# Kernel tuning notes

Measured on AMD Instinct MI355X. Metric: run time of the kernel, lower is better.

The kernel has to match this reference:

```python
import jax, jax.numpy as jnp
import numpy as np


def setup_inputs() -> dict:
    key = jax.random.key(0)
    kq, kk, kwq, kwk, kwv = jax.random.split(key, 5)
    B, T, C, H = 16, 2048, 1024, 64
    q = jax.random.normal(kq, (B, T, C), dtype=jnp.float32)
    k = jax.random.normal(kk, (B, T, C), dtype=jnp.float32)
    s = 1.0 / np.sqrt(C)
    Wq = jax.random.normal(kwq, (C, H), dtype=jnp.float32) * s
    Wk = jax.random.normal(kwk, (C, H), dtype=jnp.float32) * s
    Wv = jax.random.normal(kwv, (C, H), dtype=jnp.float32) * s
    return {"q": q, "k": k, "Wq": Wq, "Wk": Wk, "Wv": Wv}


def reference(q, k, Wq, Wk, Wv):
    # q, k: (B, T, C); projections are bias-free C -> head_size H
    Q = q @ Wq            # (B, T, H)
    K = k @ Wk            # (B, T, H)
    V = k @ Wv            # (B, T, H)
    T = q.shape[1]
    # NOTE: original scales by input dim C (q.shape[-1]), not head_size
    scale = q.shape[-1] ** (-0.5)
    wei = jnp.einsum('bth,bsh->bts', Q, K) * scale   # (B, T, T)
    causal = jnp.tril(jnp.ones((T, T), dtype=bool))
    wei = jnp.where(causal, wei, -jnp.inf)
    wei = jax.nn.softmax(wei, axis=-1)
    # dropout rate is 0.0 -> identity at inference
    out = jnp.einsum('bts,bsh->bth', wei, V)         # (B, T, H)
    return out
```

## Files before the change

### kernel.cpp

```cpp
#include <hip/hip_runtime.h>
#include <hip/hip_bf16.h>

typedef __bf16 bf16;
typedef __bf16 bf16x8 __attribute__((ext_vector_type(8)));
typedef float f32x4 __attribute__((ext_vector_type(4)));

#define MFMA_16x16x32(A, B, C) __builtin_amdgcn_mfma_f32_16x16x32_bf16(A, B, C, 0, 0, 0)

static_assert(sizeof(bf16x8) == 16, "bf16x8 must be 16B");

__global__ __launch_bounds__(256) void wtrans_kernel(
    const float* __restrict__ Wq, const float* __restrict__ Wk,
    const float* __restrict__ Wv, bf16* __restrict__ Wt)
{
  int idx = blockIdx.x * 256 + threadIdx.x;
  int p = idx >> 16;
  int rem = idx & 65535;
  int h = rem >> 10;
  int c = rem & 1023;
  const float* W = (p == 0) ? Wq : (p == 1) ? Wk : Wv;
  Wt[idx] = (bf16)W[c * 64 + h];
}

__global__ __launch_bounds__(256) void proj_kernel(
    const float* __restrict__ qin, const float* __restrict__ kin,
    const bf16* __restrict__ Wt,
    bf16* __restrict__ Qb, bf16* __restrict__ Kb, bf16* __restrict__ Vtb)
{
  const int p = blockIdx.y;
  const int m0 = blockIdx.x * 128;
  const float* A = (p == 0) ? qin : kin;
  const int nmat = (p == 0) ? 1 : 2;

  __shared__ __align__(16) bf16 Bs[2][64][80];

  const int tid = threadIdx.x;
  const int lane = tid & 63;
  const int w = tid >> 6;
  const int g = lane >> 4;
  const int r = lane & 15;

  f32x4 acc[2][2][4];
  #pragma unroll
  for (int mt = 0; mt < 2; mt++)
    #pragma unroll
    for (int rf = 0; rf < 2; rf++)
      #pragma unroll
      for (int cf = 0; cf < 4; cf++)
        acc[mt][rf][cf] = (f32x4){0.f, 0.f, 0.f, 0.f};

  const int bh = tid >> 2;
  const int bc = (tid & 3) * 16;

  for (int k0 = 0; k0 < 1024; k0 += 64) {
    #pragma unroll
    for (int mt = 0; mt < 2; mt++) {
      if (mt < nmat) {
        const bf16* src = Wt + (size_t)((p == 0) ? 0 : 1 + mt) * 65536
                          + (size_t)bh * 1024 + k0 + bc;
        *(bf16x8*)&Bs[mt][bh][bc]     = *(const bf16x8*)src;
        *(bf16x8*)&Bs[mt][bh][bc + 8] = *(const bf16x8*)(src + 8);
      }
    }
    __syncthreads();

    bf16x8 af[2][2];
    #pragma unroll
    for (int rf = 0; rf < 2; rf++) {
      const float* ap = A + (size_t)(m0 + w * 32 + rf * 16 + r) * 1024 + k0 + g * 8;
      float4 a0 = *(const float4*)(ap);
      float4 a1 = *(const float4*)(ap + 4);
      float4 a2 = *(const float4*)(ap + 32);
      float4 a3 = *(const float4*)(ap + 36);
      af[rf][0] = (bf16x8){(bf16)a0.x, (bf16)a0.y, (bf16)a0.z, (bf16)a0.w,
                           (bf16)a1.x, (bf16)a1.y, (bf16)a1.z, (bf16)a1.w};
      af[rf][1] = (bf16x8){(bf16)a2.x, (bf16)a2.y, (bf16)a2.z, (bf16)a2.w,
                           (bf16)a3.x, (bf16)a3.y, (bf16)a3.z, (bf16)a3.w};
    }

    #pragma unroll
    for (int mt = 0; mt < 2; mt++) {
      if (mt < nmat) {
        #pragma unroll
        for (int cf = 0; cf < 4; cf++) {
          bf16x8 b0 = *(const bf16x8*)&Bs[mt][cf * 16 + r][g * 8];
          bf16x8 b1 = *(const bf16x8*)&Bs[mt][cf * 16 + r][32 + g * 8];
          #pragma unroll
          for (int rf = 0; rf < 2; rf++) {
            acc[mt][rf][cf] = MFMA_16x16x32(af[rf][0], b0, acc[mt][rf][cf]);
            acc[mt][rf][cf] = MFMA_16x16x32(af[rf][1], b1, acc[mt][rf][cf]);
          }
        }
      }
    }
    __syncthreads();
  }

  #pragma unroll
  for (int rf = 0; rf < 2; rf++) {
    #pragma unroll
    for (int cf = 0; cf < 4; cf++) {
      #pragma unroll
      for (int j = 0; j < 4; j++) {
        int rg = m0 + w * 32 + rf * 16 + g * 4 + j;
        int col = cf * 16 + r;
        if (p == 0) {
          Qb[(size_t)rg * 64 + col] = (bf16)acc[0][rf][cf][j];
        } else {
          Kb[(size_t)rg * 64 + col] = (bf16)acc[0][rf][cf][j];
          int bb = rg >> 11, t = rg & 2047;
          Vtb[(size_t)(bb * 64 + col) * 2048 + t] = (bf16)acc[1][rf][cf][j];
        }
      }
    }
  }
}

__global__ __launch_bounds__(256) void attn_kernel(
    const bf16* __restrict__ Qb, const bf16* __restrict__ Kb,
    const bf16* __restrict__ Vtb, float* __restrict__ out)
{
  const int qt = (int)(gridDim.x - 1 - blockIdx.x);
  const int b = blockIdx.y;
  const int tid = threadIdx.x;
  const int lane = tid & 63;
  const int w = tid >> 6;
  const int g = lane >> 4;
  const int r = lane & 15;

  __shared__ __align__(16) bf16 Ks[64][80];
  __shared__ __align__(16) bf16 Vs[64][80];
  __shared__ __align__(16) bf16 Ps[4][16][80];

  const int q0 = qt * 64 + w * 16;
  const bf16* qp = Qb + (size_t)(b * 2048 + q0 + r) * 64 + g * 8;
  const bf16x8 qf0 = *(const bf16x8*)qp;
  const bf16x8 qf1 = *(const bf16x8*)(qp + 32);

  f32x4 acc_o[4];
  #pragma unroll
  for (int hf = 0; hf < 4; hf++) acc_o[hf] = (f32x4){0.f, 0.f, 0.f, 0.f};
  float m_r[4] = {-1e30f, -1e30f, -1e30f, -1e30f};
  float l_r[4] = {0.f, 0.f, 0.f, 0.f};
  const float scale = 0.03125f;

  const int sh = tid >> 2;
  const int sc = (tid & 3) * 16;

  for (int kv = 0; kv <= qt; kv++) {
    {
      const bf16* kp = Kb + (size_t)(b * 2048 + kv * 64 + sh) * 64 + sc;
      *(bf16x8*)&Ks[sh][sc]     = *(const bf16x8*)kp;
      *(bf16x8*)&Ks[sh][sc + 8] = *(const bf16x8*)(kp + 8);
      const bf16* vp = Vtb + (size_t)(b * 64 + sh) * 2048 + kv * 64 + sc;
      *(bf16x8*)&Vs[sh][sc]     = *(const bf16x8*)vp;
      *(bf16x8*)&Vs[sh][sc + 8] = *(const bf16x8*)(vp + 8);
    }
    __syncthreads();

    f32x4 s[4];
    #pragma unroll
    for (int cf = 0; cf < 4; cf++) {
      bf16x8 kf0 = *(const bf16x8*)&Ks[cf * 16 + r][g * 8];
      bf16x8 kf1 = *(const bf16x8*)&Ks[cf * 16 + r][32 + g * 8];
      f32x4 t = (f32x4){0.f, 0.f, 0.f, 0.f};
      t = MFMA_16x16x32(qf0, kf0, t);
      t = MFMA_16x16x32(qf1, kf1, t);
      s[cf] = t;
    }

    const bool diag = (kv == qt);
    float pm[4] = {-1e30f, -1e30f, -1e30f, -1e30f};
    #pragma unroll
    for (int cf = 0; cf < 4; cf++) {
      #pragma unroll
      for (int j = 0; j < 4; j++) {
        float v = s[cf][j] * scale;
        if (diag && (cf * 16 + r) > (w * 16 + g * 4 + j)) v = -1e30f;
        s[cf][j] = v;
        pm[j] = fmaxf(pm[j], v);
      }
    }
    #pragma unroll
    for (int j = 0; j < 4; j++) {
      #pragma unroll
      for (int msk = 1; msk < 16; msk <<= 1)
        pm[j] = fmaxf(pm[j], __shfl_xor(pm[j], msk, 64));
    }
    float corr[4];
    #pragma unroll
    for (int j = 0; j < 4; j++) {
      float mn = fmaxf(m_r[j], pm[j]);
      corr[j] = __expf(m_r[j] - mn);
      m_r[j] = mn;
    }
    float rs[4] = {0.f, 0.f, 0.f, 0.f};
    #pragma unroll
    for (int cf = 0; cf < 4; cf++) {
      #pragma unroll
      for (int j = 0; j < 4; j++) {
        float pv = __expf(s[cf][j] - m_r[j]);
        s[cf][j] = pv;
        rs[j] += pv;
      }
    }
    #pragma unroll
    for (int j = 0; j < 4; j++) {
      #pragma unroll
      for (int msk = 1; msk < 16; msk <<= 1)
        rs[j] += __shfl_xor(rs[j], msk, 64);
      l_r[j] = l_r[j] * corr[j] + rs[j];
    }
    #pragma unroll
    for (int hf = 0; hf < 4; hf++)
      #pragma unroll
      for (int j = 0; j < 4; j++)
        acc_o[hf][j] *= corr[j];

    #pragma unroll
    for (int cf = 0; cf < 4; cf++)
      #pragma unroll
      for (int j = 0; j < 4; j++)
        Ps[w][g * 4 + j][cf * 16 + r] = (bf16)s[cf][j];

    __syncthreads();

    #pragma unroll
    for (int ss = 0; ss < 2; ss++) {
      bf16x8 pf = *(const bf16x8*)&Ps[w][r][ss * 32 + g * 8];
      #pragma unroll
      for (int hf = 0; hf < 4; hf++) {
        bf16x8 vf = *(const bf16x8*)&Vs[hf * 16 + r][ss * 32 + g * 8];
        acc_o[hf] = MFMA_16x16x32(pf, vf, acc_o[hf]);
      }
    }
    __syncthreads();
  }

  float inv[4];
  #pragma unroll
  for (int j = 0; j < 4; j++) inv[j] = 1.0f / l_r[j];
  const size_t ob = (size_t)(b * 2048 + q0) * 64;
  #pragma unroll
  for (int hf = 0; hf < 4; hf++)
    #pragma unroll
    for (int j = 0; j < 4; j++)
      out[ob + (size_t)(g * 4 + j) * 64 + hf * 16 + r] = acc_o[hf][j] * inv[j];
}

extern "C" void kernel_launch(void* const* d_in, const int* in_sizes, int n_in,
                              void* d_out, int out_size, void* d_ws, size_t ws_size,
                              hipStream_t stream)
{
  const float* q  = (const float*)d_in[0];
  const float* k  = (const float*)d_in[1];
  const float* Wq = (const float*)d_in[2];
  const float* Wk = (const float*)d_in[3];
  const float* Wv = (const float*)d_in[4];
  float* out = (float*)d_out;

  char* ws = (char*)d_ws;
  bf16* Qb  = (bf16*)(ws);
  bf16* Kb  = (bf16*)(ws + (4u << 20));
  bf16* Vtb = (bf16*)(ws + (8u << 20));
  bf16* Wt  = (bf16*)(ws + (12u << 20));

  hipLaunchKernelGGL(wtrans_kernel, dim3(768), dim3(256), 0, stream,
                     Wq, Wk, Wv, Wt);
  hipLaunchKernelGGL(proj_kernel, dim3(256, 2), dim3(256), 0, stream,
                     q, k, Wt, Qb, Kb, Vtb);
  hipLaunchKernelGGL(attn_kernel, dim3(32, 16), dim3(256), 0, stream,
                     Qb, Kb, Vtb, out);
}
```

Baseline: 138.6 us.

## Drop LDS staging in projection kernel, read weights from L2, prefetch activations

The projection kernel no longer stages the transposed weights in shared memory with two barriers per k-step. Each wave now reads its B fragments straight from global memory, relying on the small 384KB weight tensor being cache-resident. Activation loads are software-prefetched one k-step ahead. Each block covers 64 rows instead of 128, and the grid is doubled to keep the same coverage. This removes the synchronisation and LDS traffic, at the cost of redundant global or L2 weight reads across all four waves.

Measured after the change: 200.7 us. +44.8%, slower.

```diff
diff --git a/kernel.cpp b/kernel.cpp
--- a/kernel.cpp
+++ b/kernel.cpp
@@ -28,11 +28,7 @@
     bf16* __restrict__ Qb, bf16* __restrict__ Kb, bf16* __restrict__ Vtb)
 {
   const int p = blockIdx.y;
-  const int m0 = blockIdx.x * 128;
-  const float* A = (p == 0) ? qin : kin;
-  const int nmat = (p == 0) ? 1 : 2;
-
-  __shared__ __align__(16) bf16 Bs[2][64][80];
+  const int m0 = blockIdx.x * 64;
 
   const int tid = threadIdx.x;
   const int lane = tid & 63;
@@ -40,77 +36,67 @@
   const int g = lane >> 4;
   const int r = lane & 15;
 
-  f32x4 acc[2][2][4];
-  #pragma unroll
-  for (int mt = 0; mt < 2; mt++)
-    #pragma unroll
-    for (int rf = 0; rf < 2; rf++)
-      #pragma unroll
-      for (int cf = 0; cf < 4; cf++)
-        acc[mt][rf][cf] = (f32x4){0.f, 0.f, 0.f, 0.f};
-
-  const int bh = tid >> 2;
-  const int bc = (tid & 3) * 16;
+  const float* A = (p == 0) ? qin : kin;
+  const float* ap_base = A + (size_t)(m0 + w * 16 + r) * 1024 + g * 8;
+
+  const bf16* W0 = Wt + (size_t)((p == 0) ? 0 : 1) * 65536 + (size_t)r * 1024 + g * 8;
+  const bf16* W1 = Wt + (size_t)2 * 65536 + (size_t)r * 1024 + g * 8;
+
+  f32x4 acc0[4], acc1[4];
+  #pragma unroll
+  for (int cf = 0; cf < 4; cf++) {
+    acc0[cf] = (f32x4){0.f, 0.f, 0.f, 0.f};
+    acc1[cf] = (f32x4){0.f, 0.f, 0.f, 0.f};
+  }
+
+  float4 a0 = *(const float4*)(ap_base);
+  float4 a1 = *(const float4*)(ap_base + 4);
+  float4 a2 = *(const float4*)(ap_base + 32);
+  float4 a3 = *(const float4*)(ap_base + 36);
 
   for (int k0 = 0; k0 < 1024; k0 += 64) {
-    #pragma unroll
-    for (int mt = 0; mt < 2; mt++) {
-      if (mt < nmat) {
-        const bf16* src = Wt + (size_t)((p == 0) ? 0 : 1 + mt) * 65536
-                          + (size_t)bh * 1024 + k0 + bc;
-        *(bf16x8*)&Bs[mt][bh][bc]     = *(const bf16x8*)src;
-        *(bf16x8*)&Bs[mt][bh][bc + 8] = *(const bf16x8*)(src + 8);
-      }
-    }
-    __syncthreads();
-
-    bf16x8 af[2][2];
-    #pragma unroll
-    for (int rf = 0; rf < 2; rf++) {
-      const float* ap = A + (size_t)(m0 + w * 32 + rf * 16 + r) * 1024 + k0 + g * 8;
-      float4 a0 = *(const float4*)(ap);
-      float4 a1 = *(const float4*)(ap + 4);
-      float4 a2 = *(const float4*)(ap + 32);
-      float4 a3 = *(const float4*)(ap + 36);
-      af[rf][0] = (bf16x8){(bf16)a0.x, (bf16)a0.y, (bf16)a0.z, (bf16)a0.w,
-                           (bf16)a1.x, (bf16)a1.y, (bf16)a1.z, (bf16)a1.w};
-      af[rf][1] = (bf16x8){(bf16)a2.x, (bf16)a2.y, (bf16)a2.z, (bf16)a2.w,
-                           (bf16)a3.x, (bf16)a3.y, (bf16)a3.z, (bf16)a3.w};
-    }
-
-    #pragma unroll
-    for (int mt = 0; mt < 2; mt++) {
-      if (mt < nmat) {
-        #pragma unroll
-        for (int cf = 0; cf < 4; cf++) {
-          bf16x8 b0 = *(const bf16x8*)&Bs[mt][cf * 16 + r][g * 8];
-          bf16x8 b1 = *(const bf16x8*)&Bs[mt][cf * 16 + r][32 + g * 8];
-          #pragma unroll
-          for (int rf = 0; rf < 2; rf++) {
-            acc[mt][rf][cf] = MFMA_16x16x32(af[rf][0], b0, acc[mt][rf][cf]);
-            acc[mt][rf][cf] = MFMA_16x16x32(af[rf][1], b1, acc[mt][rf][cf]);
-          }
-        }
-      }
-    }
-    __syncthreads();
-  }
-
-  #pragma unroll
-  for (int rf = 0; rf < 2; rf++) {
-    #pragma unroll
-    for (int cf = 0; cf < 4; cf++) {
-      #pragma unroll
-      for (int j = 0; j < 4; j++) {
-        int rg = m0 + w * 32 + rf * 16 + g * 4 + j;
-        int col = cf * 16 + r;
-        if (p == 0) {
-          Qb[(size_t)rg * 64 + col] = (bf16)acc[0][rf][cf][j];
-        } else {
-          Kb[(size_t)rg * 64 + col] = (bf16)acc[0][rf][cf][j];
-          int bb = rg >> 11, t = rg & 2047;
-          Vtb[(size_t)(bb * 64 + col) * 2048 + t] = (bf16)acc[1][rf][cf][j];
-        }
+    bf16x8 af0 = (bf16x8){(bf16)a0.x, (bf16)a0.y, (bf16)a0.z, (bf16)a0.w,
+                          (bf16)a1.x, (bf16)a1.y, (bf16)a1.z, (bf16)a1.w};
+    bf16x8 af1 = (bf16x8){(bf16)a2.x, (bf16)a2.y, (bf16)a2.z, (bf16)a2.w,
+                          (bf16)a3.x, (bf16)a3.y, (bf16)a3.z, (bf16)a3.w};
+
+    if (k0 + 64 < 1024) {
+      const float* apn = ap_base + k0 + 64;
+      a0 = *(const float4*)(apn);
+      a1 = *(const float4*)(apn + 4);
+      a2 = *(const float4*)(apn + 32);
+      a3 = *(const float4*)(apn + 36);
+    }
+
+    #pragma unroll
+    for (int cf = 0; cf < 4; cf++) {
+      const bf16* b0p = W0 + (size_t)cf * 16384 + k0;
+      bf16x8 b00 = *(const bf16x8*)(b0p);
+      bf16x8 b01 = *(const bf16x8*)(b0p + 32);
+      acc0[cf] = MFMA_16x16x32(af0, b00, acc0[cf]);
+      acc0[cf] = MFMA_16x16x32(af1, b01, acc0[cf]);
+      if (p == 1) {
+        const bf16* b1p = W1 + (size_t)cf * 16384 + k0;
+        bf16x8 b10 = *(const bf16x8*)(b1p);
+        bf16x8 b11 = *(const bf16x8*)(b1p + 32);
+        acc1[cf] = MFMA_16x16x32(af0, b10, acc1[cf]);
+        acc1[cf] = MFMA_16x16x32(af1, b11, acc1[cf]);
+      }
+    }
+  }
+
+  #pragma unroll
+  for (int cf = 0; cf < 4; cf++) {
+    #pragma unroll
+    for (int j = 0; j < 4; j++) {
+      int rg = m0 + w * 16 + g * 4 + j;
+      int col = cf * 16 + r;
+      if (p == 0) {
+        Qb[(size_t)rg * 64 + col] = (bf16)acc0[cf][j];
+      } else {
+        Kb[(size_t)rg * 64 + col] = (bf16)acc0[cf][j];
+        int bb = rg >> 11, t = rg & 2047;
+        Vtb[(size_t)(bb * 64 + col) * 2048 + t] = (bf16)acc1[cf][j];
       }
     }
   }
@@ -267,7 +253,7 @@
 
   hipLaunchKernelGGL(wtrans_kernel, dim3(768), dim3(256), 0, stream,
                      Wq, Wk, Wv, Wt);
-  hipLaunchKernelGGL(proj_kernel, dim3(256, 2), dim3(256), 0, stream,
+  hipLaunchKernelGGL(proj_kernel, dim3(512, 2), dim3(256), 0, stream,
                      q, k, Wt, Qb, Kb, Vtb);
   hipLaunchKernelGGL(attn_kernel, dim3(32, 16), dim3(256), 0, stream,
                      Qb, Kb, Vtb, out);
```

## Double-buffer projection GEMM tiles via async global-to-LDS loads

Applied to the files above, without the earlier changes.

The projection kernel now stages both the fp32 activation tile and the bf16 weight tile into shared memory with direct global-to-LDS loads, double-buffered at a K-step of 32, so the next tile is fetched while MFMAs run on the current one. This removes the per-iteration register round trip and one barrier per step, and the launch bounds now ask for two blocks per CU. The cost is more LDS use (two 16KB fp32 A buffers) and unpadded LDS layouts that may cause bank conflicts on the fragment reads. The attention kernel, which likely dominates the runtime, is untouched.

Result: faster. 127.9 us (-7.7%).

```diff
diff --git a/kernel.cpp b/kernel.cpp
--- a/kernel.cpp
+++ b/kernel.cpp
@@ -8,6 +8,12 @@
 #define MFMA_16x16x32(A, B, C) __builtin_amdgcn_mfma_f32_16x16x32_bf16(A, B, C, 0, 0, 0)
 
 static_assert(sizeof(bf16x8) == 16, "bf16x8 must be 16B");
+
+__device__ __forceinline__ void gld16(void* lds, const void* g) {
+  __builtin_amdgcn_global_load_lds(
+      (const __attribute__((address_space(1))) unsigned int*)g,
+      (__attribute__((address_space(3))) unsigned int*)lds, 16, 0, 0);
+}
 
 __global__ __launch_bounds__(256) void wtrans_kernel(
     const float* __restrict__ Wq, const float* __restrict__ Wk,
@@ -22,7 +28,7 @@
   Wt[idx] = (bf16)W[c * 64 + h];
 }
 
-__global__ __launch_bounds__(256) void proj_kernel(
+__global__ __launch_bounds__(256, 2) void proj_kernel(
     const float* __restrict__ qin, const float* __restrict__ kin,
     const bf16* __restrict__ Wt,
     bf16* __restrict__ Qb, bf16* __restrict__ Kb, bf16* __restrict__ Vtb)
@@ -32,7 +38,8 @@
   const float* A = (p == 0) ? qin : kin;
   const int nmat = (p == 0) ? 1 : 2;
 
-  __shared__ __align__(16) bf16 Bs[2][64][80];
+  __shared__ __align__(16) float As[2][128 * 32];
+  __shared__ __align__(16) bf16  Bs[2][2][64 * 32];
 
   const int tid = threadIdx.x;
   const int lane = tid & 63;
@@ -49,33 +56,42 @@
       for (int cf = 0; cf < 4; cf++)
         acc[mt][rf][cf] = (f32x4){0.f, 0.f, 0.f, 0.f};
 
-  const int bh = tid >> 2;
-  const int bc = (tid & 3) * 16;
-
-  for (int k0 = 0; k0 < 1024; k0 += 64) {
+  const int brow = tid >> 2;
+  const int bch = tid & 3;
+
+  auto stage = [&](int buf, int k0) {
+    #pragma unroll
+    for (int i = 0; i < 4; i++) {
+      int ci = i * 256 + tid;
+      int row = ci >> 3, ch = ci & 7;
+      gld16(&As[buf][ci * 4],
+            A + (size_t)(m0 + row) * 1024 + k0 + ch * 4);
+    }
     #pragma unroll
     for (int mt = 0; mt < 2; mt++) {
       if (mt < nmat) {
         const bf16* src = Wt + (size_t)((p == 0) ? 0 : 1 + mt) * 65536
-                          + (size_t)bh * 1024 + k0 + bc;
-        *(bf16x8*)&Bs[mt][bh][bc]     = *(const bf16x8*)src;
-        *(bf16x8*)&Bs[mt][bh][bc + 8] = *(const bf16x8*)(src + 8);
-      }
-    }
-    __syncthreads();
-
-    bf16x8 af[2][2];
+                          + (size_t)brow * 1024 + k0 + bch * 8;
+        gld16(&Bs[buf][mt][(size_t)tid * 8], src);
+      }
+    }
+  };
+
+  stage(0, 0);
+
+  for (int it = 0; it < 32; ++it) {
+    const int cur = it & 1;
+    __syncthreads();
+    if (it + 1 < 32) stage(cur ^ 1, (it + 1) * 32);
+
+    bf16x8 af[2];
     #pragma unroll
     for (int rf = 0; rf < 2; rf++) {
-      const float* ap = A + (size_t)(m0 + w * 32 + rf * 16 + r) * 1024 + k0 + g * 8;
-      float4 a0 = *(const float4*)(ap);
-      float4 a1 = *(const float4*)(ap + 4);
-      float4 a2 = *(const float4*)(ap + 32);
-      float4 a3 = *(const float4*)(ap + 36);
-      af[rf][0] = (bf16x8){(bf16)a0.x, (bf16)a0.y, (bf16)a0.z, (bf16)a0.w,
-                           (bf16)a1.x, (bf16)a1.y, (bf16)a1.z, (bf16)a1.w};
-      af[rf][1] = (bf16x8){(bf16)a2.x, (bf16)a2.y, (bf16)a2.z, (bf16)a2.w,
-                           (bf16)a3.x, (bf16)a3.y, (bf16)a3.z, (bf16)a3.w};
+      const float* ap = &As[cur][(w * 32 + rf * 16 + r) * 32 + g * 8];
+      float4 lo = *(const float4*)ap;
+      float4 hi = *(const float4*)(ap + 4);
+      af[rf] = (bf16x8){(bf16)lo.x, (bf16)lo.y, (bf16)lo.z, (bf16)lo.w,
+                        (bf16)hi.x, (bf16)hi.y, (bf16)hi.z, (bf16)hi.w};
     }
 
     #pragma unroll
@@ -83,17 +99,13 @@
       if (mt < nmat) {
         #pragma unroll
         for (int cf = 0; cf < 4; cf++) {
-          bf16x8 b0 = *(const bf16x8*)&Bs[mt][cf * 16 + r][g * 8];
-          bf16x8 b1 = *(const bf16x8*)&Bs[mt][cf * 16 + r][32 + g * 8];
+          bf16x8 bfr = *(const bf16x8*)&Bs[cur][mt][(cf * 16 + r) * 32 + g * 8];
           #pragma unroll
-          for (int rf = 0; rf < 2; rf++) {
-            acc[mt][rf][cf] = MFMA_16x16x32(af[rf][0], b0, acc[mt][rf][cf]);
-            acc[mt][rf][cf] = MFMA_16x16x32(af[rf][1], b1, acc[mt][rf][cf]);
-          }
+          for (int rf = 0; rf < 2; rf++)
+            acc[mt][rf][cf] = MFMA_16x16x32(af[rf], bfr, acc[mt][rf][cf]);
         }
       }
     }
-    __syncthreads();
   }
 
   #pragma unroll
```

## Software-pipeline projection GEMM with triple-buffered LDS and register prefetch

Applied to the files above, without the earlier changes.

Rewrites the projection kernel's K loop as a software pipeline. Global loads of A (fp32 activations) and B (bf16 weights) are issued two 32-wide K steps ahead into registers, and weights are staged through a triple-buffered LDS ring. A single raw lgkmcnt wait plus barrier replaces the two __syncthreads per iteration. The grid is flattened so q and k blocks interleave. The aim is to hide HBM latency in the memory-bound projection, which reads 256MB of fp32 input. The cost is more registers and fragile hand-written waitcnt synchronisation.

After: 137.9 us. Within noise of the previous version (-0.5%).

```diff
diff --git a/kernel.cpp b/kernel.cpp
--- a/kernel.cpp
+++ b/kernel.cpp
@@ -8,6 +8,11 @@
 #define MFMA_16x16x32(A, B, C) __builtin_amdgcn_mfma_f32_16x16x32_bf16(A, B, C, 0, 0, 0)
 
 static_assert(sizeof(bf16x8) == 16, "bf16x8 must be 16B");
+
+__device__ __forceinline__ bf16x8 cast8(float4 lo, float4 hi) {
+  return (bf16x8){(bf16)lo.x, (bf16)lo.y, (bf16)lo.z, (bf16)lo.w,
+                  (bf16)hi.x, (bf16)hi.y, (bf16)hi.z, (bf16)hi.w};
+}
 
 __global__ __launch_bounds__(256) void wtrans_kernel(
     const float* __restrict__ Wq, const float* __restrict__ Wk,
@@ -27,18 +32,27 @@
     const bf16* __restrict__ Wt,
     bf16* __restrict__ Qb, bf16* __restrict__ Kb, bf16* __restrict__ Vtb)
 {
-  const int p = blockIdx.y;
-  const int m0 = blockIdx.x * 128;
-  const float* A = (p == 0) ? qin : kin;
-  const int nmat = (p == 0) ? 1 : 2;
-
-  __shared__ __align__(16) bf16 Bs[2][64][80];
+  const int bid = blockIdx.x;
+  const int p = bid & 1;
+  const int m0 = (bid >> 1) * 128;
+  const float* A = p ? kin : qin;
+
+  __shared__ __align__(16) bf16 Bsh[3][2][64][40];
 
   const int tid = threadIdx.x;
   const int lane = tid & 63;
   const int w = tid >> 6;
   const int g = lane >> 4;
   const int r = lane & 15;
+  const int row16 = lane >> 2;
+  const int q4 = lane & 3;
+
+  const float* aA = A + (size_t)(m0 + w * 32 + r) * 1024 + g * 8;
+  const float* aB = aA + 16 * 1024;
+
+  const bf16* wbase = Wt + (size_t)(w * 16 + row16) * 1024 + q4 * 8;
+  const bf16* bp0 = wbase + (size_t)(p ? 1 : 0) * 65536;
+  const bf16* bp1 = wbase + (size_t)2 * 65536;
 
   f32x4 acc[2][2][4];
   #pragma unroll
@@ -49,67 +63,98 @@
       for (int cf = 0; cf < 4; cf++)
         acc[mt][rf][cf] = (f32x4){0.f, 0.f, 0.f, 0.f};
 
-  const int bh = tid >> 2;
-  const int bc = (tid & 3) * 16;
-
-  for (int k0 = 0; k0 < 1024; k0 += 64) {
-    #pragma unroll
-    for (int mt = 0; mt < 2; mt++) {
-      if (mt < nmat) {
-        const bf16* src = Wt + (size_t)((p == 0) ? 0 : 1 + mt) * 65536
-                          + (size_t)bh * 1024 + k0 + bc;
-        *(bf16x8*)&Bs[mt][bh][bc]     = *(const bf16x8*)src;
-        *(bf16x8*)&Bs[mt][bh][bc + 8] = *(const bf16x8*)(src + 8);
-      }
-    }
-    __syncthreads();
-
-    bf16x8 af[2][2];
-    #pragma unroll
-    for (int rf = 0; rf < 2; rf++) {
-      const float* ap = A + (size_t)(m0 + w * 32 + rf * 16 + r) * 1024 + k0 + g * 8;
-      float4 a0 = *(const float4*)(ap);
-      float4 a1 = *(const float4*)(ap + 4);
-      float4 a2 = *(const float4*)(ap + 32);
-      float4 a3 = *(const float4*)(ap + 36);
-      af[rf][0] = (bf16x8){(bf16)a0.x, (bf16)a0.y, (bf16)a0.z, (bf16)a0.w,
-                           (bf16)a1.x, (bf16)a1.y, (bf16)a1.z, (bf16)a1.w};
-      af[rf][1] = (bf16x8){(bf16)a2.x, (bf16)a2.y, (bf16)a2.z, (bf16)a2.w,
-                           (bf16)a3.x, (bf16)a3.y, (bf16)a3.z, (bf16)a3.w};
-    }
-
-    #pragma unroll
-    for (int mt = 0; mt < 2; mt++) {
-      if (mt < nmat) {
-        #pragma unroll
-        for (int cf = 0; cf < 4; cf++) {
-          bf16x8 b0 = *(const bf16x8*)&Bs[mt][cf * 16 + r][g * 8];
-          bf16x8 b1 = *(const bf16x8*)&Bs[mt][cf * 16 + r][32 + g * 8];
-          #pragma unroll
-          for (int rf = 0; rf < 2; rf++) {
-            acc[mt][rf][cf] = MFMA_16x16x32(af[rf][0], b0, acc[mt][rf][cf]);
-            acc[mt][rf][cf] = MFMA_16x16x32(af[rf][1], b1, acc[mt][rf][cf]);
-          }
-        }
-      }
-    }
-    __syncthreads();
+  float4 A1a0, A2a0, A1b0, A2b0, A1a1, A2a1, A1b1, A2b1;
+  bf16x8 B00, B10, B01, B11;
+
+#define ISSA(S, K)                                                       \
+  do {                                                                   \
+    A1a##S = *(const float4*)(aA + (K));                                 \
+    A2a##S = *(const float4*)(aA + (K) + 4);                             \
+    A1b##S = *(const float4*)(aB + (K));                                 \
+    A2b##S = *(const float4*)(aB + (K) + 4);                             \
+  } while (0)
+
+#define ISSB(S, K)                                                       \
+  do {                                                                   \
+    B0##S = *(const bf16x8*)(bp0 + (K));                                 \
+    if (p) B1##S = *(const bf16x8*)(bp1 + (K));                          \
+  } while (0)
+
+#define WRB(S, BUF)                                                      \
+  do {                                                                   \
+    *(bf16x8*)&Bsh[BUF][0][w * 16 + row16][q4 * 8] = B0##S;              \
+    if (p) *(bf16x8*)&Bsh[BUF][1][w * 16 + row16][q4 * 8] = B1##S;       \
+  } while (0)
+
+#define LGKM_BARRIER() \
+  asm volatile("s_waitcnt lgkmcnt(0)\n\ts_barrier" ::: "memory")
+
+  auto compute = [&](float4 l1a, float4 l2a, float4 l1b, float4 l2b,
+                     int bufR) {
+    bf16x8 af0 = cast8(l1a, l2a);
+    bf16x8 af1 = cast8(l1b, l2b);
+    #pragma unroll
+    for (int cf = 0; cf < 4; cf++) {
+      bf16x8 b0 = *(const bf16x8*)&Bsh[bufR][0][cf * 16 + r][g * 8];
+      acc[0][0][cf] = MFMA_16x16x32(af0, b0, acc[0][0][cf]);
+      acc[0][1][cf] = MFMA_16x16x32(af1, b0, acc[0][1][cf]);
+    }
+    if (p) {
+      #pragma unroll
+      for (int cf = 0; cf < 4; cf++) {
+        bf16x8 b1 = *(const bf16x8*)&Bsh[bufR][1][cf * 16 + r][g * 8];
+        acc[1][0][cf] = MFMA_16x16x32(af0, b1, acc[1][0][cf]);
+        acc[1][1][cf] = MFMA_16x16x32(af1, b1, acc[1][1][cf]);
+      }
+    }
+  };
+
+  ISSA(0, 0);  ISSB(0, 0);
+  ISSA(1, 32); ISSB(1, 32);
+  WRB(0, 0);
+  ISSB(0, 64);
+  LGKM_BARRIER();
+
+  int bufW = 1, bufR = 0;
+  for (int j = 0; j < 16; ++j) {
+    const int t0 = 2 * j, t1 = 2 * j + 1;
+
+    WRB(1, bufW);
+    if (t0 + 3 < 32) ISSB(1, (t0 + 3) * 32);
+    LGKM_BARRIER();
+    compute(A1a0, A2a0, A1b0, A2b0, bufR);
+    if (t0 + 2 < 32) ISSA(0, (t0 + 2) * 32);
+    bufW = (bufW == 2) ? 0 : bufW + 1;
+    bufR = (bufR == 2) ? 0 : bufR + 1;
+
+    if (t1 + 1 < 32) WRB(0, bufW);
+    if (t1 + 3 < 32) ISSB(0, (t1 + 3) * 32);
+    LGKM_BARRIER();
+    compute(A1a1, A2a1, A1b1, A2b1, bufR);
+    if (t1 + 2 < 32) ISSA(1, (t1 + 2) * 32);
+    bufW = (bufW == 2) ? 0 : bufW + 1;
+    bufR = (bufR == 2) ? 0 : bufR + 1;
   }
 
+#undef ISSA
+#undef ISSB
+#undef WRB
+#undef LGKM_BARRIER
+
   #pragma unroll
   for (int rf = 0; rf < 2; rf++) {
     #pragma unroll
     for (int cf = 0; cf < 4; cf++) {
       #pragma unroll
-      for (int j = 0; j < 4; j++) {
-        int rg = m0 + w * 32 + rf * 16 + g * 4 + j;
+      for (int jj = 0; jj < 4; jj++) {
+        int rg = m0 + w * 32 + rf * 16 + g * 4 + jj;
         int col = cf * 16 + r;
         if (p == 0) {
-          Qb[(size_t)rg * 64 + col] = (bf16)acc[0][rf][cf][j];
+          Qb[(size_t)rg * 64 + col] = (bf16)acc[0][rf][cf][jj];
         } else {
-          Kb[(size_t)rg * 64 + col] = (bf16)acc[0][rf][cf][j];
-          int bb = rg >> 11, t = rg & 2047;
-          Vtb[(size_t)(bb * 64 + col) * 2048 + t] = (bf16)acc[1][rf][cf][j];
+          Kb[(size_t)rg * 64 + col] = (bf16)acc[0][rf][cf][jj];
+          int bb = rg >> 11, t2 = rg & 2047;
+          Vtb[(size_t)(bb * 64 + col) * 2048 + t2] = (bf16)acc[1][rf][cf][jj];
         }
       }
     }
@@ -267,7 +312,7 @@
 
   hipLaunchKernelGGL(wtrans_kernel, dim3(768), dim3(256), 0, stream,
                      Wq, Wk, Wv, Wt);
-  hipLaunchKernelGGL(proj_kernel, dim3(256, 2), dim3(256), 0, stream,
+  hipLaunchKernelGGL(proj_kernel, dim3(512), dim3(256), 0, stream,
                      q, k, Wt, Qb, Kb, Vtb);
   hipLaunchKernelGGL(attn_kernel, dim3(32, 16), dim3(256), 0, stream,
                      Qb, Kb, Vtb, out);
```
